# Performance work log

Measured on AMD Instinct MI355X. Metric: run time of the kernel, lower is better.

## Reference

```python
import jax, jax.numpy as jnp
import numpy as np

N, E, D, G, OUT, K = 150000, 1200000, 128, 512, 2, 2
EPS = 1e-5


def setup_inputs() -> dict:
    key = jax.random.key(0)
    ks = jax.random.split(key, 8)
    nfeat = jax.random.normal(ks[0], (N, D), dtype=jnp.float32)
    src = jax.random.randint(ks[1], (E,), 0, N, dtype=jnp.int32)
    dst = jax.random.randint(ks[2], (E,), 0, N, dtype=jnp.int32)
    node2graph = jnp.sort(jax.random.randint(ks[3], (N,), 0, G, dtype=jnp.int32))
    s = 1.0 / np.sqrt(D)
    conv_w = jax.random.normal(ks[4], (D, D), dtype=jnp.float32) * s
    conv_b = jnp.zeros((D,), jnp.float32)
    gamma1 = jnp.ones((D,), jnp.float32)
    beta1 = jnp.zeros((D,), jnp.float32)
    gamma2 = jnp.ones((D,), jnp.float32)
    beta2 = jnp.zeros((D,), jnp.float32)
    pred_w = jax.random.normal(ks[5], (D, OUT), dtype=jnp.float32) * s
    pred_b = jnp.zeros((OUT,), jnp.float32)
    return {"nfeat": nfeat, "src": src, "dst": dst, "node2graph": node2graph,
            "num_graphs": G,
            "conv_w": conv_w, "conv_b": conv_b,
            "gamma1": gamma1, "beta1": beta1,
            "gamma2": gamma2, "beta2": beta2,
            "pred_w": pred_w, "pred_b": pred_b}


def _batchnorm(h, gamma, beta):
    # batch-norm over the node dimension (training-mode stats)
    mu = jnp.mean(h, axis=0)
    var = jnp.mean(jnp.square(h - mu), axis=0)
    return (h - mu) * jax.lax.rsqrt(var + EPS) * gamma + beta


def reference(nfeat, src, dst, node2graph, num_graphs,
              conv_w, conv_b, gamma1, beta1, gamma2, beta2, pred_w, pred_b):
    n = nfeat.shape[0]
    # symmetric degree normalization D^{-1/2} A D^{-1/2}
    deg = jax.ops.segment_sum(jnp.ones_like(dst, dtype=nfeat.dtype), dst, num_segments=n)
    dnorm = jax.lax.rsqrt(jnp.clip(deg, 1.0, None))  # [N]
    h = nfeat  # dropout with p=0 is identity
    for _ in range(K):  # k-hop SGC propagation interleaved with norm
        m = (h * dnorm[:, None])[src]                       # [E, D] gather
        h = jax.ops.segment_sum(m, dst, num_segments=n)     # scatter-add
        h = h * dnorm[:, None]
        h = _batchnorm(h, gamma1, beta1)
    h = h @ conv_w + conv_b          # SGConv linear
    h = _batchnorm(h, gamma2, beta2)  # middle norm
    h = jax.nn.relu(h)                # activation (dropout p=0)
    # mean pooling per graph
    cnt = jax.ops.segment_sum(jnp.ones((n,), h.dtype), node2graph, num_segments=num_graphs)
    g = jax.ops.segment_sum(h, node2graph, num_segments=num_graphs)
    g = g / jnp.clip(cnt, 1.0, None)[:, None]
    return g @ pred_w + pred_b  # [G, OUT]
```

## Files before the change

kernel.cpp:

```cpp
#include <hip/hip_runtime.h>
#include <hip/hip_fp16.h>
#include <cstddef>
#include <cstdint>

constexpr int DIMS = 128;
constexpr float BN_EPS = 1e-5f;
constexpr int NSH = 64;
constexpr int GB = 2048;
constexpr int NPB = 512;

typedef _Float16 f16x8 __attribute__((ext_vector_type(8)));
typedef float f32x4 __attribute__((ext_vector_type(4)));

static __device__ __forceinline__ f16x8 as_f16x8(uint4 u) {
  union { uint4 u; f16x8 h; } x; x.u = u; return x.h;
}
static __device__ __forceinline__ __half2 as_h2(uint32_t u) {
  union { uint32_t u; __half2 h; } x; x.u = u; return x.h;
}
static __device__ __forceinline__ uint32_t h2bits(__half2 h) {
  union { __half2 h; uint32_t u; } x; x.h = h; return x.u;
}

__global__ void zero_k(float* __restrict__ fp, size_t nf) {
  size_t i = (size_t)blockIdx.x * blockDim.x + threadIdx.x;
  if (i < nf) fp[i] = 0.f;
}

__global__ void cvt_k(const float4* __restrict__ in4, uint2* __restrict__ out,
                      const float* __restrict__ dnorm, size_t n32) {
  size_t i = (size_t)blockIdx.x * blockDim.x + threadIdx.x;
  size_t stride = (size_t)gridDim.x * blockDim.x;
  for (; i < n32; i += stride) {
    float d = dnorm[i >> 5];
    float4 v = in4[i];
    __half2 h0 = __floats2half2_rn(v.x * d, v.y * d);
    __half2 h1 = __floats2half2_rn(v.z * d, v.w * d);
    out[i] = make_uint2(h2bits(h0), h2bits(h1));
  }
}


__global__ __launch_bounds__(256) void cnt_k(const int* __restrict__ dst,
                                             int* __restrict__ C, int e, int chunk) {
  __shared__ int hist[512];
  int b = blockIdx.x;
  for (int j = threadIdx.x; j < 512; j += 256) hist[j] = 0;
  __syncthreads();
  int i0 = b * chunk;
  int i1 = i0 + chunk; if (i1 > e) i1 = e;
  for (int i = i0 + threadIdx.x; i < i1; i += 256)
    atomicAdd(&hist[dst[i] >> 9], 1);
  __syncthreads();
  for (int j = threadIdx.x; j < 512; j += 256) C[b * 512 + j] = hist[j];
}

__global__ __launch_bounds__(512) void colscan_k(int* __restrict__ C, int* __restrict__ tot) {
  int j = blockIdx.x;
  int t = threadIdx.x;
  int v = C[t * 512 + j];
  __shared__ int lds[512];
  lds[t] = v; __syncthreads();
  for (int off = 1; off < 512; off <<= 1) {
    int add = (t >= off) ? lds[t - off] : 0;
    __syncthreads();
    lds[t] += add;
    __syncthreads();
  }
  C[t * 512 + j] = lds[t] - v;
  if (t == 511) tot[j] = lds[511];
}

__global__ __launch_bounds__(512) void bscan_k(const int* __restrict__ tot, int nbins,
                                               int* __restrict__ boff, int* __restrict__ adj,
                                               int e) {
  int t = threadIdx.x;
  int v = tot[t];
  __shared__ int lds[512];
  lds[t] = v; __syncthreads();
  for (int off = 1; off < 512; off <<= 1) {
    int add = (t >= off) ? lds[t - off] : 0;
    __syncthreads();
    lds[t] += add;
    __syncthreads();
  }
  boff[t] = lds[t] - v;
  if (t == 0) boff[nbins] = e;
  if (t < 8) adj[e + t] = 0;
}

__global__ __launch_bounds__(512) void scat_k(const int* __restrict__ src,
                                              const int* __restrict__ dst,
                                              const int* __restrict__ C,
                                              const int* __restrict__ boff,
                                              int* __restrict__ ebin, int e, int chunk) {
  __shared__ int cur[512];
  int b = blockIdx.x;
  int t = threadIdx.x;
  cur[t] = boff[t] + C[b * 512 + t];
  __syncthreads();
  int i0 = b * chunk;
  int i1 = i0 + chunk; if (i1 > e) i1 = e;
  for (int i = i0 + t; i < i1; i += 512) {
    int d = dst[i];
    int bin = d >> 9;
    int p = atomicAdd(&cur[bin], 1);
    ebin[p] = (src[i] << 9) | (d & 511);
  }
}

__global__ __launch_bounds__(512) void binidx_k(
    const int* __restrict__ ebin, const int* __restrict__ boff,
    int* __restrict__ row_off, float* __restrict__ dnorm, int n, int nbins) {
  __shared__ int cnt[512];
  __shared__ int scn[512];
  int b = blockIdx.x;
  int t = threadIdx.x;
  cnt[t] = 0;
  __syncthreads();
  int j0 = boff[b], j1 = boff[b + 1];
  for (int i = j0 + t; i < j1; i += 512) atomicAdd(&cnt[ebin[i] & 511], 1);
  __syncthreads();
  int v = cnt[t];
  scn[t] = v; __syncthreads();
  for (int off = 1; off < 512; off <<= 1) {
    int add = (t >= off) ? scn[t - off] : 0;
    __syncthreads();
    scn[t] += add;
    __syncthreads();
  }
  int node = (b << 9) + t;
  if (node < n) {
    row_off[node] = j0 + scn[t] - v;
    dnorm[node] = rsqrtf(fmaxf((float)v, 1.0f));
  }
  if (b == nbins - 1 && t == 0) row_off[n] = j1;
}

__global__ __launch_bounds__(512) void adj_bins_k(
    const int* __restrict__ ebin, const int* __restrict__ boff,
    const int* __restrict__ row_off, const float* __restrict__ dnorm,
    int* __restrict__ adj, float* __restrict__ wsum, int n) {
  __shared__ int cur[512];
  __shared__ int ro[512];
  __shared__ float ws[512];
  int b = blockIdx.x;
  int base = b << 9;
  int t = threadIdx.x;
  {
    cur[t] = 0;
    ws[t] = 0.f;
    int node = base + t;
    ro[t] = (node < n) ? row_off[node] : 0;
  }
  __syncthreads();
  int j0 = boff[b], j1 = boff[b + 1];
  for (int i = j0 + t; i < j1; i += 512) {
    int pk = ebin[i];
    int dl = pk & 511;
    int s = pk >> 9;
    int p = atomicAdd(&cur[dl], 1);
    adj[ro[dl] + p] = s;
    atomicAdd(&ws[dl], dnorm[s]);
  }
  __syncthreads();
  {
    int node = base + t;
    if (node < n) wsum[node] = ws[t];
  }
}

template <bool AFF>
__global__ __launch_bounds__(256) void gather_k(
    const uint32_t* __restrict__ Xu, uint32_t* __restrict__ Yout,
    const int* __restrict__ row_off, const int* __restrict__ adj,
    const float* __restrict__ dn, const float* __restrict__ wsum,
    const float* __restrict__ a, const float* __restrict__ b,
    float* __restrict__ sumS, float* __restrict__ sqS, int n, int nwaves) {
  int tid = threadIdx.x;
  int l = tid & 63, w = tid >> 6;
  int wid = blockIdx.x * 4 + w;
  uint32_t lu = (uint32_t)l;
  int f0 = 2 * l;
  float af0 = 1.f, bf0 = 0.f, af1 = 1.f, bf1 = 0.f;
  if (AFF) { af0 = a[f0]; bf0 = b[f0]; af1 = a[f0 + 1]; bf1 = b[f0 + 1]; }
  float s0 = 0.f, s1 = 0.f, q0 = 0.f, q1 = 0.f;

  for (int nodeA = wid; nodeA < n; nodeA += 2 * nwaves) {
    const int nodeB = nodeA + nwaves;
    const bool hasB = nodeB < n;
    int ja = row_off[nodeA];
    const int ea = row_off[nodeA + 1];
    int jb = hasB ? row_off[nodeB] : 0;
    const int eb = hasB ? row_off[nodeB + 1] : 0;
    float accA0 = 0.f, accA1 = 0.f, accB0 = 0.f, accB1 = 0.f;

    while ((ja < ea) || (jb < eb)) {
      uint32_t xa[8], xb[8];
      const bool runA = ja < ea, runB = jb < eb;
      if (runA) {
#pragma unroll
        for (int t = 0; t < 8; ++t) {
          int jj = ja + t;
          uint32_t sj = (uint32_t)adj[jj];
          uint32_t v = Xu[(sj << 6) + lu];
          xa[t] = (jj < ea) ? v : 0u;
        }
      }
      if (runB) {
#pragma unroll
        for (int t = 0; t < 8; ++t) {
          int jj = jb + t;
          uint32_t sj = (uint32_t)adj[jj];
          uint32_t v = Xu[(sj << 6) + lu];
          xb[t] = (jj < eb) ? v : 0u;
        }
      }
      if (runA) {
        __half2 t0 = __hadd2(as_h2(xa[0]), as_h2(xa[1]));
        __half2 t1 = __hadd2(as_h2(xa[2]), as_h2(xa[3]));
        __half2 t2 = __hadd2(as_h2(xa[4]), as_h2(xa[5]));
        __half2 t3 = __hadd2(as_h2(xa[6]), as_h2(xa[7]));
        float2 u0 = __half22float2(__hadd2(t0, t1));
        float2 u1 = __half22float2(__hadd2(t2, t3));
        accA0 += u0.x + u1.x;
        accA1 += u0.y + u1.y;
        ja += 8;
      }
      if (runB) {
        __half2 t0 = __hadd2(as_h2(xb[0]), as_h2(xb[1]));
        __half2 t1 = __hadd2(as_h2(xb[2]), as_h2(xb[3]));
        __half2 t2 = __hadd2(as_h2(xb[4]), as_h2(xb[5]));
        __half2 t3 = __hadd2(as_h2(xb[6]), as_h2(xb[7]));
        float2 u0 = __half22float2(__hadd2(t0, t1));
        float2 u1 = __half22float2(__hadd2(t2, t3));
        accB0 += u0.x + u1.x;
        accB1 += u0.y + u1.y;
        jb += 8;
      }
    }

    {
      float dnn = dn[nodeA];
      float v0, v1;
      if constexpr (AFF) {
        float wsn = wsum[nodeA];
        v0 = dnn * fmaf(af0, accA0, bf0 * wsn);
        v1 = dnn * fmaf(af1, accA1, bf1 * wsn);
        __half2 hv = __floats2half2_rn(v0, v1);
        Yout[((uint32_t)nodeA << 6) + lu] = h2bits(hv);
      } else {
        v0 = dnn * accA0;
        v1 = dnn * accA1;
        __half2 hv = __floats2half2_rn(v0 * dnn, v1 * dnn);
        Yout[((uint32_t)nodeA << 6) + lu] = h2bits(hv);
      }
      s0 += v0; s1 += v1; q0 += v0 * v0; q1 += v1 * v1;
    }
    if (hasB) {
      float dnn = dn[nodeB];
      float v0, v1;
      if constexpr (AFF) {
        float wsn = wsum[nodeB];
        v0 = dnn * fmaf(af0, accB0, bf0 * wsn);
        v1 = dnn * fmaf(af1, accB1, bf1 * wsn);
        __half2 hv = __floats2half2_rn(v0, v1);
        Yout[((uint32_t)nodeB << 6) + lu] = h2bits(hv);
      } else {
        v0 = dnn * accB0;
        v1 = dnn * accB1;
        __half2 hv = __floats2half2_rn(v0 * dnn, v1 * dnn);
        Yout[((uint32_t)nodeB << 6) + lu] = h2bits(hv);
      }
      s0 += v0; s1 += v1; q0 += v0 * v0; q1 += v1 * v1;
    }
  }

  __shared__ float red[4][256];
  red[w][l] = s0; red[w][64 + l] = s1; red[w][128 + l] = q0; red[w][192 + l] = q1;
  __syncthreads();
  float t = red[0][tid] + red[1][tid] + red[2][tid] + red[3][tid];
  int comp = tid >> 6, li = tid & 63;
  int sh = blockIdx.x & (NSH - 1);
  float* dstp = ((comp & 2) ? sqS : sumS) + sh * DIMS;
  atomicAdd(&dstp[2 * li + (comp & 1)], t);
}

__global__ void affine_k(const float* __restrict__ sum, const float* __restrict__ sq,
                         const float* __restrict__ gamma, const float* __restrict__ beta,
                         float* __restrict__ a, float* __restrict__ b, float invn) {
  int d = threadIdx.x;
  float s = 0.f, q = 0.f;
  for (int k = 0; k < NSH; ++k) { s += sum[k * DIMS + d]; q += sq[k * DIMS + d]; }
  float mu = s * invn;
  float var = q * invn - mu * mu;
  float rs = rsqrtf(var + BN_EPS);
  float ad = rs * gamma[d];
  a[d] = ad;
  b[d] = beta[d] - mu * ad;
}

__global__ void foldw_k(const float* __restrict__ W, const float* __restrict__ cb,
                        const float* __restrict__ a2, const float* __restrict__ b2,
                        __half* __restrict__ Wt, float* __restrict__ cp) {
  int o = blockIdx.x;
  int d = threadIdx.x;
  float w = W[d * DIMS + o];
  Wt[o * DIMS + d] = __float2half(a2[d] * w);
  __shared__ float red[128];
  red[d] = b2[d] * w;
  __syncthreads();
  for (int off = 64; off > 0; off >>= 1) {
    if (d < off) red[d] += red[d + off];
    __syncthreads();
  }
  if (d == 0) cp[o] = red[0] + cb[o];
}

__global__ __launch_bounds__(256) void matmul_k(
    const uint4* __restrict__ X, const uint4* __restrict__ Wt,
    const float* __restrict__ cp, uint4* __restrict__ Z,
    float* __restrict__ sumS, float* __restrict__ sqS, int n) {
  int tid = threadIdx.x;
  int l = tid & 63, w = tid >> 6;
  int rowg = l & 15;
  int kg = l >> 4;
  int r0 = (blockIdx.x * 4 + w) * 32;
  bool active = r0 < n;

  __shared__ __half outs[4][16][136];
  __shared__ float sred[4][128], qred[4][128];
  float svals[8], qvals[8];

  if (active) {
    f32x4 acc0[8] = {}, acc1[8] = {};
    const uint4* xr0 = X + (size_t)(r0 + rowg) * 16;
    const uint4* xr1 = X + (size_t)(r0 + 16 + rowg) * 16;
    bool ok0 = (r0 + rowg) < n;
    bool ok1 = (r0 + 16 + rowg) < n;
#pragma unroll
    for (int kk = 0; kk < 4; ++kk) {
      uint4 au0 = ok0 ? xr0[kk * 4 + kg] : make_uint4(0u, 0u, 0u, 0u);
      uint4 au1 = ok1 ? xr1[kk * 4 + kg] : make_uint4(0u, 0u, 0u, 0u);
      f16x8 a0 = as_f16x8(au0), a1 = as_f16x8(au1);
#pragma unroll
      for (int c = 0; c < 8; ++c) {
        f16x8 bfr = as_f16x8(Wt[(size_t)(c * 16 + rowg) * 16 + kk * 4 + kg]);
        acc0[c] = __builtin_amdgcn_mfma_f32_16x16x32_f16(a0, bfr, acc0[c], 0, 0, 0);
        acc1[c] = __builtin_amdgcn_mfma_f32_16x16x32_f16(a1, bfr, acc1[c], 0, 0, 0);
      }
    }
#pragma unroll
    for (int c = 0; c < 8; ++c) { svals[c] = 0.f; qvals[c] = 0.f; }
#pragma unroll
    for (int gidx = 0; gidx < 2; ++gidx) {
      int rbase = r0 + gidx * 16;
#pragma unroll
      for (int c = 0; c < 8; ++c) {
        float cpv = cp[c * 16 + rowg];
        f32x4 av = (gidx == 0) ? acc0[c] : acc1[c];
#pragma unroll
        for (int r = 0; r < 4; ++r) {
          int row = rbase + kg * 4 + r;
          float vv = av[r] + cpv;
          vv = (row < n) ? vv : 0.f;
          svals[c] += vv; qvals[c] += vv * vv;
          outs[w][kg * 4 + r][c * 16 + rowg] = __float2half(vv);
        }
      }
#pragma unroll
      for (int it = 0; it < 4; ++it) {
        int lr = it * 4 + kg;
        int grow = rbase + lr;
        if (grow < n)
          Z[(size_t)grow * 16 + rowg] = *(const uint4*)&outs[w][lr][rowg * 8];
      }
    }
#pragma unroll
    for (int c = 0; c < 8; ++c) {
      svals[c] += __shfl_xor(svals[c], 16); svals[c] += __shfl_xor(svals[c], 32);
      qvals[c] += __shfl_xor(qvals[c], 16); qvals[c] += __shfl_xor(qvals[c], 32);
    }
  }
  if (active) {
    if (kg == 0) {
#pragma unroll
      for (int c = 0; c < 8; ++c) {
        sred[w][c * 16 + rowg] = svals[c];
        qred[w][c * 16 + rowg] = qvals[c];
      }
    }
  } else {
    sred[w][l] = 0.f; sred[w][64 + l] = 0.f;
    qred[w][l] = 0.f; qred[w][64 + l] = 0.f;
  }
  __syncthreads();
  int f = tid & 127;
  int sh = blockIdx.x & (NSH - 1);
  if (tid < 128) {
    float s = sred[0][f] + sred[1][f] + sred[2][f] + sred[3][f];
    atomicAdd(&sumS[sh * DIMS + f], s);
  } else {
    float q = qred[0][f] + qred[1][f] + qred[2][f] + qred[3][f];
    atomicAdd(&sqS[sh * DIMS + f], q);
  }
}

__global__ void gstart_k(const int* __restrict__ n2g, int* __restrict__ gstart, int n, int G) {
  int i = blockIdx.x * blockDim.x + threadIdx.x;
  if (i >= n) return;
  int g = n2g[i];
  int gp = (i == 0) ? -1 : n2g[i - 1];
  for (int x = gp + 1; x <= g; ++x) gstart[x] = i;
  if (i == n - 1) {
    for (int x = g + 1; x <= G; ++x) gstart[x] = n;
  }
}

__global__ __launch_bounds__(512) void pool_pred_k(
    const uint4* __restrict__ Z, const int* __restrict__ gstart,
    const float* __restrict__ a3, const float* __restrict__ b3,
    const float* __restrict__ pw, const float* __restrict__ pb,
    float* __restrict__ out) {
  int g = blockIdx.x;
  int tid = threadIdx.x;
  int l = tid & 63, w = tid >> 6;
  int grp = l >> 4, fl = l & 15;
  int f0 = fl * 8;
  float av[8], bv[8];
#pragma unroll
  for (int q = 0; q < 8; ++q) { av[q] = a3[f0 + q]; bv[q] = b3[f0 + q]; }
  int s = gstart[g], e = gstart[g + 1];
  float rs[8] = {0.f, 0.f, 0.f, 0.f, 0.f, 0.f, 0.f, 0.f};
  for (int ni = s + (w * 4 + grp); ni < e; ni += 32) {
    uint4 zv = Z[(size_t)ni * 16 + fl];
    const __half2* h = (const __half2*)&zv;
#pragma unroll
    for (int q = 0; q < 4; ++q) {
      float2 z = __half22float2(h[q]);
      rs[2 * q] += fmaxf(fmaf(z.x, av[2 * q], bv[2 * q]), 0.f);
      rs[2 * q + 1] += fmaxf(fmaf(z.y, av[2 * q + 1], bv[2 * q + 1]), 0.f);
    }
  }
  float p0 = 0.f, p1 = 0.f;
#pragma unroll
  for (int q = 0; q < 8; ++q) {
    p0 += rs[q] * pw[(f0 + q) * 2 + 0];
    p1 += rs[q] * pw[(f0 + q) * 2 + 1];
  }
  __shared__ float r[2][512];
  r[0][tid] = p0; r[1][tid] = p1;
  __syncthreads();
  for (int off = 256; off > 0; off >>= 1) {
    if (tid < off) { r[0][tid] += r[0][tid + off]; r[1][tid] += r[1][tid + off]; }
    __syncthreads();
  }
  if (tid == 0) {
    float inv = 1.f / fmaxf((float)(e - s), 1.f);
    out[g * 2 + 0] = r[0][0] * inv + pb[0];
    out[g * 2 + 1] = r[1][0] * inv + pb[1];
  }
}

extern "C" void kernel_launch(void* const* d_in, const int* in_sizes, int n_in,
                              void* d_out, int out_size, void* d_ws, size_t ws_size,
                              hipStream_t stream) {
  const float* nfeat  = (const float*)d_in[0];
  const int*   src    = (const int*)d_in[1];
  const int*   dst    = (const int*)d_in[2];
  const int*   n2g    = (const int*)d_in[3];
  const float* conv_w = (const float*)d_in[5];
  const float* conv_b = (const float*)d_in[6];
  const float* gamma1 = (const float*)d_in[7];
  const float* beta1  = (const float*)d_in[8];
  const float* gamma2 = (const float*)d_in[9];
  const float* beta2  = (const float*)d_in[10];
  const float* pred_w = (const float*)d_in[11];
  const float* pred_b = (const float*)d_in[12];
  float* out = (float*)d_out;
  (void)n_in; (void)ws_size;

  const int n = in_sizes[0] / DIMS;
  const int e = in_sizes[1];
  const int g = out_size / 2;
  const int nbins = (n + 511) >> 9;

  char* p = (char*)d_ws;
  auto alloc = [&](size_t bytes) { char* r = p; p += (bytes + 255) & ~(size_t)255; return r; };
  uint32_t* Xp  = (uint32_t*)alloc((size_t)n * 64 * 4);
  uint32_t* W1  = (uint32_t*)alloc((size_t)n * 64 * 4);
  uint32_t* Y2  = (uint32_t*)alloc((size_t)n * 64 * 4);
  __half*   Zh  = (__half*)alloc((size_t)n * 64 * 4);
  float* dnorm = (float*)alloc((size_t)n * 4);
  float* stat  = (float*)alloc(((size_t)6 * NSH * DIMS + n) * 4);
  float* wsum  = stat + 6 * NSH * DIMS;
  float* affA  = (float*)alloc(3 * DIMS * 4);
  float* affB  = (float*)alloc(3 * DIMS * 4);
  __half* Wt   = (__half*)alloc(DIMS * DIMS * 2);
  float* cp    = (float*)alloc(DIMS * 4);
  int* row_off = (int*)alloc(((size_t)n + 1) * 4);
  int* adj     = (int*)alloc(((size_t)e + 8) * 4);
  int* ebin    = (int*)alloc((size_t)e * 4);
  int* Cmat    = (int*)alloc((size_t)NPB * 512 * 4);
  int* tot     = (int*)alloc(512 * 4);
  int* boff    = (int*)alloc(520 * 4);
  int* gstart  = (int*)alloc(((size_t)g + 1) * 4);

  const int SLAB = NSH * DIMS;
  float* S0 = stat + 0 * SLAB; float* Q0 = stat + 1 * SLAB;
  float* S1 = stat + 2 * SLAB; float* Q1 = stat + 3 * SLAB;
  float* S2 = stat + 4 * SLAB; float* Q2 = stat + 5 * SLAB;

  const float invn = 1.0f / (float)n;
  const int nwaves = GB * 4;
  const int chunk = (e + NPB - 1) / NPB;

  zero_k<<<dim3(((size_t)6 * SLAB + 255) / 256), dim3(256), 0, stream>>>(stat, (size_t)6 * SLAB);
  cnt_k<<<dim3(NPB), dim3(256), 0, stream>>>(dst, Cmat, e, chunk);
  colscan_k<<<dim3(512), dim3(512), 0, stream>>>(Cmat, tot);
  bscan_k<<<dim3(1), dim3(512), 0, stream>>>(tot, nbins, boff, adj, e);
  scat_k<<<dim3(NPB), dim3(512), 0, stream>>>(src, dst, Cmat, boff, ebin, e, chunk);
  binidx_k<<<dim3(nbins), dim3(512), 0, stream>>>(ebin, boff, row_off, dnorm, n, nbins);
  cvt_k<<<dim3(2048), dim3(256), 0, stream>>>((const float4*)nfeat, (uint2*)Xp, dnorm,
                                              (size_t)n * 32);
  adj_bins_k<<<dim3(nbins), dim3(512), 0, stream>>>(ebin, boff, row_off, dnorm, adj, wsum, n);

  gather_k<false><<<dim3(GB), dim3(256), 0, stream>>>(
      Xp, W1, row_off, adj, dnorm, wsum, nullptr, nullptr, S0, Q0, n, nwaves);
  affine_k<<<dim3(1), dim3(DIMS), 0, stream>>>(S0, Q0, gamma1, beta1, affA + 0, affB + 0, invn);
  gather_k<true><<<dim3(GB), dim3(256), 0, stream>>>(
      W1, Y2, row_off, adj, dnorm, wsum, affA + 0, affB + 0, S1, Q1, n, nwaves);
  affine_k<<<dim3(1), dim3(DIMS), 0, stream>>>(S1, Q1, gamma1, beta1, affA + DIMS, affB + DIMS, invn);
  foldw_k<<<dim3(DIMS), dim3(DIMS), 0, stream>>>(conv_w, conv_b, affA + DIMS, affB + DIMS, Wt, cp);
  matmul_k<<<dim3((n + 127) / 128), dim3(256), 0, stream>>>(
      (const uint4*)Y2, (const uint4*)Wt, cp, (uint4*)Zh, S2, Q2, n);
  affine_k<<<dim3(1), dim3(DIMS), 0, stream>>>(S2, Q2, gamma2, beta2, affA + 2 * DIMS, affB + 2 * DIMS, invn);
  gstart_k<<<dim3((n + 255) / 256), dim3(256), 0, stream>>>(n2g, gstart, n, g);
  pool_pred_k<<<dim3(g), dim3(512), 0, stream>>>((const uint4*)Zh, gstart,
                                                 affA + 2 * DIMS, affB + 2 * DIMS,
                                                 pred_w, pred_b, out);
}
```

Baseline: 265.9 us.

## Split neighbor gather into two feature-half passes with half-wave edge parallelism

The gather kernel is templated on a feature pass, so each launch processes 64 of the 128 features. Within a wave, two 32-lane halves take alternating edges and combine their sums with a cross-half shuffle. This halves the random-access working set of each pass so gathered rows are more likely to stay cached, at the cost of re-reading adjacency and launching twice as many gather kernels. The grid size is also doubled, and the adjacency padding grows to cover 16-edge strides.

```diff
diff --git a/kernel.cpp b/kernel.cpp
--- a/kernel.cpp
+++ b/kernel.cpp
@@ -6,7 +6,7 @@
 constexpr int DIMS = 128;
 constexpr float BN_EPS = 1e-5f;
 constexpr int NSH = 64;
-constexpr int GB = 2048;
+constexpr int GB = 4096;
 constexpr int NPB = 512;
 
 typedef _Float16 f16x8 __attribute__((ext_vector_type(8)));
@@ -86,7 +86,7 @@
   }
   boff[t] = lds[t] - v;
   if (t == 0) boff[nbins] = e;
-  if (t < 8) adj[e + t] = 0;
+  if (t < 16) adj[e + t] = 0;
 }
 
 __global__ __launch_bounds__(512) void scat_k(const int* __restrict__ src,
@@ -170,7 +170,7 @@
   }
 }
 
-template <bool AFF>
+template <bool AFF, int PASS>
 __global__ __launch_bounds__(256) void gather_k(
     const uint32_t* __restrict__ Xu, uint32_t* __restrict__ Yout,
     const int* __restrict__ row_off, const int* __restrict__ adj,
@@ -180,8 +180,10 @@
   int tid = threadIdx.x;
   int l = tid & 63, w = tid >> 6;
   int wid = blockIdx.x * 4 + w;
-  uint32_t lu = (uint32_t)l;
-  int f0 = 2 * l;
+  int lg = l >> 5;
+  uint32_t fl = (uint32_t)(l & 31);
+  const uint32_t XOFF = PASS * 32;
+  int f0 = PASS * 64 + 2 * (int)fl;
   float af0 = 1.f, bf0 = 0.f, af1 = 1.f, bf1 = 0.f;
   if (AFF) { af0 = a[f0]; bf0 = b[f0]; af1 = a[f0 + 1]; bf1 = b[f0 + 1]; }
   float s0 = 0.f, s1 = 0.f, q0 = 0.f, q1 = 0.f;
@@ -201,18 +203,20 @@
       if (runA) {
 #pragma unroll
         for (int t = 0; t < 8; ++t) {
-          int jj = ja + t;
-          uint32_t sj = (uint32_t)adj[jj];
-          uint32_t v = Xu[(sj << 6) + lu];
+          int jj = ja + 2 * t + lg;
+          int jc = jj < ea ? jj : ea - 1;
+          uint32_t sj = (uint32_t)adj[jc];
+          uint32_t v = Xu[(sj << 6) + XOFF + fl];
           xa[t] = (jj < ea) ? v : 0u;
         }
       }
       if (runB) {
 #pragma unroll
         for (int t = 0; t < 8; ++t) {
-          int jj = jb + t;
-          uint32_t sj = (uint32_t)adj[jj];
-          uint32_t v = Xu[(sj << 6) + lu];
+          int jj = jb + 2 * t + lg;
+          int jc = jj < eb ? jj : eb - 1;
+          uint32_t sj = (uint32_t)adj[jc];
+          uint32_t v = Xu[(sj << 6) + XOFF + fl];
           xb[t] = (jj < eb) ? v : 0u;
         }
       }
@@ -225,7 +229,7 @@
         float2 u1 = __half22float2(__hadd2(t2, t3));
         accA0 += u0.x + u1.x;
         accA1 += u0.y + u1.y;
-        ja += 8;
+        ja += 16;
       }
       if (runB) {
         __half2 t0 = __hadd2(as_h2(xb[0]), as_h2(xb[1]));
@@ -236,8 +240,15 @@
         float2 u1 = __half22float2(__hadd2(t2, t3));
         accB0 += u0.x + u1.x;
         accB1 += u0.y + u1.y;
-        jb += 8;
-      }
+        jb += 16;
+      }
+    }
+
+    accA0 += __shfl_xor(accA0, 32);
+    accA1 += __shfl_xor(accA1, 32);
+    if (hasB) {
+      accB0 += __shfl_xor(accB0, 32);
+      accB1 += __shfl_xor(accB1, 32);
     }
 
     {
@@ -247,13 +258,14 @@
         float wsn = wsum[nodeA];
         v0 = dnn * fmaf(af0, accA0, bf0 * wsn);
         v1 = dnn * fmaf(af1, accA1, bf1 * wsn);
-        __half2 hv = __floats2half2_rn(v0, v1);
-        Yout[((uint32_t)nodeA << 6) + lu] = h2bits(hv);
+        if (lg == 0)
+          Yout[((uint32_t)nodeA << 6) + XOFF + fl] = h2bits(__floats2half2_rn(v0, v1));
       } else {
         v0 = dnn * accA0;
         v1 = dnn * accA1;
-        __half2 hv = __floats2half2_rn(v0 * dnn, v1 * dnn);
-        Yout[((uint32_t)nodeA << 6) + lu] = h2bits(hv);
+        if (lg == 0)
+          Yout[((uint32_t)nodeA << 6) + XOFF + fl] =
+              h2bits(__floats2half2_rn(v0 * dnn, v1 * dnn));
       }
       s0 += v0; s1 += v1; q0 += v0 * v0; q1 += v1 * v1;
     }
@@ -264,26 +276,35 @@
         float wsn = wsum[nodeB];
         v0 = dnn * fmaf(af0, accB0, bf0 * wsn);
         v1 = dnn * fmaf(af1, accB1, bf1 * wsn);
-        __half2 hv = __floats2half2_rn(v0, v1);
-        Yout[((uint32_t)nodeB << 6) + lu] = h2bits(hv);
+        if (lg == 0)
+          Yout[((uint32_t)nodeB << 6) + XOFF + fl] = h2bits(__floats2half2_rn(v0, v1));
       } else {
         v0 = dnn * accB0;
         v1 = dnn * accB1;
-        __half2 hv = __floats2half2_rn(v0 * dnn, v1 * dnn);
-        Yout[((uint32_t)nodeB << 6) + lu] = h2bits(hv);
+        if (lg == 0)
+          Yout[((uint32_t)nodeB << 6) + XOFF + fl] =
+              h2bits(__floats2half2_rn(v0 * dnn, v1 * dnn));
       }
       s0 += v0; s1 += v1; q0 += v0 * v0; q1 += v1 * v1;
     }
   }
 
-  __shared__ float red[4][256];
-  red[w][l] = s0; red[w][64 + l] = s1; red[w][128 + l] = q0; red[w][192 + l] = q1;
-  __syncthreads();
-  float t = red[0][tid] + red[1][tid] + red[2][tid] + red[3][tid];
-  int comp = tid >> 6, li = tid & 63;
-  int sh = blockIdx.x & (NSH - 1);
-  float* dstp = ((comp & 2) ? sqS : sumS) + sh * DIMS;
-  atomicAdd(&dstp[2 * li + (comp & 1)], t);
+  __shared__ float red[4][128];
+  if (lg == 0) {
+    red[w][0 * 32 + fl] = s0;
+    red[w][1 * 32 + fl] = s1;
+    red[w][2 * 32 + fl] = q0;
+    red[w][3 * 32 + fl] = q1;
+  }
+  __syncthreads();
+  if (tid < 128) {
+    float v = red[0][tid] + red[1][tid] + red[2][tid] + red[3][tid];
+    int comp = tid >> 5, fs = tid & 31;
+    int f = PASS * 64 + 2 * fs + (comp & 1);
+    float* dstp = (comp & 2) ? sqS : sumS;
+    int sh = blockIdx.x & (NSH - 1);
+    atomicAdd(&dstp[sh * DIMS + f], v);
+  }
 }
 
 __global__ void affine_k(const float* __restrict__ sum, const float* __restrict__ sq,
@@ -499,7 +520,7 @@
   __half* Wt   = (__half*)alloc(DIMS * DIMS * 2);
   float* cp    = (float*)alloc(DIMS * 4);
   int* row_off = (int*)alloc(((size_t)n + 1) * 4);
-  int* adj     = (int*)alloc(((size_t)e + 8) * 4);
+  int* adj     = (int*)alloc(((size_t)e + 16) * 4);
   int* ebin    = (int*)alloc((size_t)e * 4);
   int* Cmat    = (int*)alloc((size_t)NPB * 512 * 4);
   int* tot     = (int*)alloc(512 * 4);
@@ -525,10 +546,14 @@
                                               (size_t)n * 32);
   adj_bins_k<<<dim3(nbins), dim3(512), 0, stream>>>(ebin, boff, row_off, dnorm, adj, wsum, n);
 
-  gather_k<false><<<dim3(GB), dim3(256), 0, stream>>>(
+  gather_k<false, 0><<<dim3(GB), dim3(256), 0, stream>>>(
+      Xp, W1, row_off, adj, dnorm, wsum, nullptr, nullptr, S0, Q0, n, nwaves);
+  gather_k<false, 1><<<dim3(GB), dim3(256), 0, stream>>>(
       Xp, W1, row_off, adj, dnorm, wsum, nullptr, nullptr, S0, Q0, n, nwaves);
   affine_k<<<dim3(1), dim3(DIMS), 0, stream>>>(S0, Q0, gamma1, beta1, affA + 0, affB + 0, invn);
-  gather_k<true><<<dim3(GB), dim3(256), 0, stream>>>(
+  gather_k<true, 0><<<dim3(GB), dim3(256), 0, stream>>>(
+      W1, Y2, row_off, adj, dnorm, wsum, affA + 0, affB + 0, S1, Q1, n, nwaves);
+  gather_k<true, 1><<<dim3(GB), dim3(256), 0, stream>>>(
       W1, Y2, row_off, adj, dnorm, wsum, affA + 0, affB + 0, S1, Q1, n, nwaves);
   affine_k<<<dim3(1), dim3(DIMS), 0, stream>>>(S1, Q1, gamma1, beta1, affA + DIMS, affB + DIMS, invn);
   foldw_k<<<dim3(DIMS), dim3(DIMS), 0, stream>>>(conv_w, conv_b, affA + DIMS, affB + DIMS, Wt, cp);
```

After: 293.4 us. 1.1x slower.
